# Kernel tuning notes

Hardware: AMD Instinct MI355X
Metric: run time of the kernel (lower is better)

## Reference

```python
import jax, jax.numpy as jnp
import numpy as np

D = 4096   # dim_context == dim_hid
A = 10     # dim_out (agent feature vector)
EPS = 1e-5


def _ln(x, g, b):
    mu = jnp.mean(x)
    var = jnp.mean((x - mu) ** 2)
    return (x - mu) / jnp.sqrt(var + EPS) * g + b


def _mlp3(x, W0, b0, g0, be0, W1, b1, g1, be1, W2, b2):
    # Linear -> LayerNorm -> ReLU, twice, then final Linear
    h = jax.nn.relu(_ln(W0 @ x + b0, g0, be0))
    h = jax.nn.relu(_ln(W1 @ h + b1, g1, be1))
    return W2 @ h + b2


def _lin_init(key, d_out, d_in):
    s = 1.0 / np.sqrt(d_in)
    return jax.random.uniform(key, (d_out, d_in), jnp.float32, -s, s)


def setup_inputs() -> dict:
    key = jax.random.key(0)
    ks = jax.random.split(key, 24)
    inp = {
        "context_vec": jax.random.normal(ks[0], (D,), jnp.float32),
        "prev_hidden": jax.random.normal(ks[1], (D,), jnp.float32),
        "attn_scores": jax.random.normal(ks[2], (D,), jnp.float32),
        "prev_agent_feat": jax.random.normal(ks[3], (A,), jnp.float32),
        # input_mlp: (A+D) -> D -> D -> D
        "in_W0": _lin_init(ks[4], D, A + D), "in_b0": jnp.zeros((D,), jnp.float32),
        "in_g0": jnp.ones((D,), jnp.float32), "in_be0": jnp.zeros((D,), jnp.float32),
        "in_W1": _lin_init(ks[5], D, D), "in_b1": jnp.zeros((D,), jnp.float32),
        "in_g1": jnp.ones((D,), jnp.float32), "in_be1": jnp.zeros((D,), jnp.float32),
        "in_W2": _lin_init(ks[6], D, D), "in_b2": jnp.zeros((D,), jnp.float32),
        # GRUCell (gate order: r, z, n)
        "gru_Wih": _lin_init(ks[7], 3 * D, D), "gru_Whh": _lin_init(ks[8], 3 * D, D),
        "gru_bih": jnp.zeros((3 * D,), jnp.float32), "gru_bhh": jnp.zeros((3 * D,), jnp.float32),
        # out_mlp: D -> D -> D -> A
        "out_W0": _lin_init(ks[9], D, D), "out_b0": jnp.zeros((D,), jnp.float32),
        "out_g0": jnp.ones((D,), jnp.float32), "out_be0": jnp.zeros((D,), jnp.float32),
        "out_W1": _lin_init(ks[10], D, D), "out_b1": jnp.zeros((D,), jnp.float32),
        "out_g1": jnp.ones((D,), jnp.float32), "out_be1": jnp.zeros((D,), jnp.float32),
        "out_W2": _lin_init(ks[11], A, D), "out_b2": jnp.zeros((A,), jnp.float32),
    }
    return inp


def _forward(context_vec, prev_hidden, attn_scores, prev_agent_feat,
             in_W0, in_b0, in_g0, in_be0, in_W1, in_b1, in_g1, in_be1, in_W2, in_b2,
             gru_Wih, gru_Whh, gru_bih, gru_bhh,
             out_W0, out_b0, out_g0, out_be0, out_W1, out_b1, out_g1, out_be1, out_W2, out_b2):
    attn_w = jax.nn.softmax(attn_scores)
    gru_in = jnp.concatenate([attn_w * context_vec, prev_agent_feat])  # [D+A]
    gru_in = jax.nn.relu(_mlp3(gru_in, in_W0, in_b0, in_g0, in_be0,
                               in_W1, in_b1, in_g1, in_be1, in_W2, in_b2))
    # GRUCell
    gi = gru_Wih @ gru_in + gru_bih
    gh = gru_Whh @ prev_hidden + gru_bhh
    r = jax.nn.sigmoid(gi[:D] + gh[:D])
    z = jax.nn.sigmoid(gi[D:2 * D] + gh[D:2 * D])
    n = jnp.tanh(gi[2 * D:] + r * gh[2 * D:])
    hidden = (1.0 - z) * n + z * prev_hidden
    out = _mlp3(hidden, out_W0, out_b0, out_g0, out_be0,
                out_W1, out_b1, out_g1, out_be1, out_W2, out_b2)
    agent_feat = jnp.concatenate([
        out[0:2],
        out[2:4] / jnp.linalg.norm(out[2:4]),
        jax.nn.softplus(out[4:7]),
        jax.nn.softmax(out[7:10]),
    ])
    return agent_feat, hidden


def reference(context_vec, prev_hidden, attn_scores, prev_agent_feat,
              in_W0, in_b0, in_g0, in_be0, in_W1, in_b1, in_g1, in_be1, in_W2, in_b2,
              gru_Wih, gru_Whh, gru_bih, gru_bhh,
              out_W0, out_b0, out_g0, out_be0, out_W1, out_b1, out_g1, out_be1, out_W2, out_b2):
    return _forward(context_vec, prev_hidden, attn_scores, prev_agent_feat,
                    in_W0, in_b0, in_g0, in_be0, in_W1, in_b1, in_g1, in_be1, in_W2, in_b2,
                    gru_Wih, gru_Whh, gru_bih, gru_bhh,
                    out_W0, out_b0, out_g0, out_be0, out_W1, out_b1, out_g1, out_be1, out_W2, out_b2)
```

## Files before the change

### kernel.cpp

```cpp
#include <hip/hip_runtime.h>
#include <math.h>

#define D 4096
#define DA 4106

__device__ __forceinline__ float wave_reduce_sum(float v) {
    #pragma unroll
    for (int off = 32; off > 0; off >>= 1) v += __shfl_xor(v, off, 64);
    return v;
}
__device__ __forceinline__ float wave_reduce_max(float v) {
    #pragma unroll
    for (int off = 32; off > 0; off >>= 1) v = fmaxf(v, __shfl_xor(v, off, 64));
    return v;
}

__global__ __launch_bounds__(1024)
void prep_kernel(const float* __restrict__ attn, const float* __restrict__ ctx,
                 const float* __restrict__ paf, float* __restrict__ gin) {
    __shared__ float red[16];
    __shared__ float bmax, bsum;
    int tid = threadIdx.x, wave = tid >> 6, lane = tid & 63;

    float4 a = ((const float4*)attn)[tid];
    float mx = fmaxf(fmaxf(a.x, a.y), fmaxf(a.z, a.w));
    mx = wave_reduce_max(mx);
    if (lane == 0) red[wave] = mx;
    __syncthreads();
    if (tid == 0) {
        float m = red[0];
        #pragma unroll
        for (int k = 1; k < 16; ++k) m = fmaxf(m, red[k]);
        bmax = m;
    }
    __syncthreads();
    mx = bmax;

    float e0 = expf(a.x - mx), e1 = expf(a.y - mx), e2 = expf(a.z - mx), e3 = expf(a.w - mx);
    float s = wave_reduce_sum(e0 + e1 + e2 + e3);
    __syncthreads();
    if (lane == 0) red[wave] = s;
    __syncthreads();
    if (tid == 0) {
        float t = 0.f;
        #pragma unroll
        for (int k = 0; k < 16; ++k) t += red[k];
        bsum = t;
    }
    __syncthreads();
    float inv = 1.f / bsum;

    float4 c = ((const float4*)ctx)[tid];
    float4 o;
    o.x = e0 * inv * c.x; o.y = e1 * inv * c.y; o.z = e2 * inv * c.z; o.w = e3 * inv * c.w;
    ((float4*)gin)[tid] = o;
    if (tid < 10) gin[D + tid] = paf[tid];
}

template<int NC, bool LN_IN, bool RELU_OUT, int RPW>
__global__ __launch_bounds__(256)
void gemv_kernel(const float* __restrict__ W, const float* __restrict__ xin,
                 const float* __restrict__ bias,
                 const float* __restrict__ g, const float* __restrict__ be,
                 float* __restrict__ y) {
    __shared__ float xs[4160];
    __shared__ float red[8];
    int tid = threadIdx.x, wave = tid >> 6, lane = tid & 63;

    if constexpr (LN_IN) {
        const float4* x4 = (const float4*)xin;
        float4 vals[4];
        float s1 = 0.f, s2 = 0.f;
        #pragma unroll
        for (int k = 0; k < 4; ++k) {
            float4 v = x4[tid + k * 256];
            vals[k] = v;
            s1 += (v.x + v.y) + (v.z + v.w);
            s2 += (v.x * v.x + v.y * v.y) + (v.z * v.z + v.w * v.w);
        }
        s1 = wave_reduce_sum(s1); s2 = wave_reduce_sum(s2);
        if (lane == 0) { red[wave] = s1; red[4 + wave] = s2; }
        __syncthreads();
        float ts1 = (red[0] + red[1]) + (red[2] + red[3]);
        float ts2 = (red[4] + red[5]) + (red[6] + red[7]);
        float mu = ts1 * (1.f / 4096.f);
        float rstd = rsqrtf(ts2 * (1.f / 4096.f) - mu * mu + 1e-5f);
        #pragma unroll
        for (int k = 0; k < 4; ++k) {
            float4 v = vals[k];
            float4 gg = ((const float4*)g)[tid + k * 256];
            float4 bb = ((const float4*)be)[tid + k * 256];
            float4 o;
            o.x = fmaxf((v.x - mu) * rstd * gg.x + bb.x, 0.f);
            o.y = fmaxf((v.y - mu) * rstd * gg.y + bb.y, 0.f);
            o.z = fmaxf((v.z - mu) * rstd * gg.z + bb.z, 0.f);
            o.w = fmaxf((v.w - mu) * rstd * gg.w + bb.w, 0.f);
            ((float4*)xs)[tid + k * 256] = o;
        }
        __syncthreads();
    } else {
        for (int i = tid; i < (NC >> 1); i += 256)
            ((float2*)xs)[i] = ((const float2*)xin)[i];
        __syncthreads();
    }

    int row0 = (blockIdx.x * 4 + wave) * RPW;
    if constexpr ((NC & 255) == 0) {
        constexpr int NIT = NC >> 8;
        const float4* xs4 = (const float4*)xs;
        for (int rr = 0; rr < RPW; ++rr) {
            int row = row0 + rr;
            const float4* Wr = (const float4*)(W + (size_t)row * NC);
            float ax = 0.f, ay = 0.f, az = 0.f, aw = 0.f;
            #pragma unroll 8
            for (int it = 0; it < NIT; ++it) {
                float4 w = Wr[it * 64 + lane];
                float4 xv = xs4[it * 64 + lane];
                ax += w.x * xv.x; ay += w.y * xv.y; az += w.z * xv.z; aw += w.w * xv.w;
            }
            float s = wave_reduce_sum((ax + ay) + (az + aw));
            if (lane == 0) {
                s += bias[row];
                if (RELU_OUT) s = fmaxf(s, 0.f);
                y[row] = s;
            }
        }
    } else {
        constexpr int NC2 = NC >> 1;
        constexpr int NFULL = NC2 >> 6;
        const float2* xs2 = (const float2*)xs;
        for (int rr = 0; rr < RPW; ++rr) {
            int row = row0 + rr;
            const float2* Wr = (const float2*)(W + (size_t)row * NC);
            float ax = 0.f, ay = 0.f;
            #pragma unroll 8
            for (int it = 0; it < NFULL; ++it) {
                float2 w = Wr[it * 64 + lane];
                float2 xv = xs2[it * 64 + lane];
                ax += w.x * xv.x; ay += w.y * xv.y;
            }
            int idx = (NFULL << 6) + lane;
            if (idx < NC2) {
                float2 w = Wr[idx];
                float2 xv = xs2[idx];
                ax += w.x * xv.x; ay += w.y * xv.y;
            }
            float s = wave_reduce_sum(ax + ay);
            if (lane == 0) {
                s += bias[row];
                if (RELU_OUT) s = fmaxf(s, 0.f);
                y[row] = s;
            }
        }
    }
}

template<int RPW>
__global__ __launch_bounds__(256)
void gru_gemv_kernel(const float* __restrict__ Wih, const float* __restrict__ Whh,
                     const float* __restrict__ xa, const float* __restrict__ xb,
                     const float* __restrict__ bih, const float* __restrict__ bhh,
                     float* __restrict__ gi, float* __restrict__ gh) {
    __shared__ float xsa[D], xsb[D];
    int tid = threadIdx.x, wave = tid >> 6, lane = tid & 63;
    for (int i = tid; i < 1024; i += 256) {
        ((float4*)xsa)[i] = ((const float4*)xa)[i];
        ((float4*)xsb)[i] = ((const float4*)xb)[i];
    }
    __syncthreads();

    const float4* xa4 = (const float4*)xsa;
    const float4* xb4 = (const float4*)xsb;
    int row0 = (blockIdx.x * 4 + wave) * RPW;
    for (int rr = 0; rr < RPW; ++rr) {
        int row = row0 + rr;
        {
            const float4* Wr = (const float4*)(Wih + (size_t)row * D);
            float ax = 0.f, ay = 0.f, az = 0.f, aw = 0.f;
            #pragma unroll 8
            for (int it = 0; it < 16; ++it) {
                float4 w = Wr[it * 64 + lane];
                float4 xv = xa4[it * 64 + lane];
                ax += w.x * xv.x; ay += w.y * xv.y; az += w.z * xv.z; aw += w.w * xv.w;
            }
            float s = wave_reduce_sum((ax + ay) + (az + aw));
            if (lane == 0) gi[row] = s + bih[row];
        }
        {
            const float4* Wr = (const float4*)(Whh + (size_t)row * D);
            float ax = 0.f, ay = 0.f, az = 0.f, aw = 0.f;
            #pragma unroll 8
            for (int it = 0; it < 16; ++it) {
                float4 w = Wr[it * 64 + lane];
                float4 xv = xb4[it * 64 + lane];
                ax += w.x * xv.x; ay += w.y * xv.y; az += w.z * xv.z; aw += w.w * xv.w;
            }
            float s = wave_reduce_sum((ax + ay) + (az + aw));
            if (lane == 0) gh[row] = s + bhh[row];
        }
    }
}

__global__ __launch_bounds__(256)
void gru_combine_kernel(const float* __restrict__ gi, const float* __restrict__ gh,
                        const float* __restrict__ hprev,
                        float* __restrict__ hidden, float* __restrict__ out_hidden) {
    int j = blockIdx.x * 256 + threadIdx.x;
    float r = 1.f / (1.f + expf(-(gi[j] + gh[j])));
    float z = 1.f / (1.f + expf(-(gi[D + j] + gh[D + j])));
    float n = tanhf(gi[2 * D + j] + r * gh[2 * D + j]);
    float h = (1.f - z) * n + z * hprev[j];
    hidden[j] = h;
    out_hidden[j] = h;
}

__global__ __launch_bounds__(1024)
void final_kernel(const float* __restrict__ t4, const float* __restrict__ g,
                  const float* __restrict__ be, const float* __restrict__ W2,
                  const float* __restrict__ b2, float* __restrict__ dout) {
    __shared__ float xs[D];
    __shared__ float red[32];
    __shared__ float out10[10];
    int tid = threadIdx.x, wave = tid >> 6, lane = tid & 63;

    float4 v = ((const float4*)t4)[tid];
    float s1 = (v.x + v.y) + (v.z + v.w);
    float s2 = (v.x * v.x + v.y * v.y) + (v.z * v.z + v.w * v.w);
    s1 = wave_reduce_sum(s1); s2 = wave_reduce_sum(s2);
    if (lane == 0) { red[wave] = s1; red[16 + wave] = s2; }
    __syncthreads();
    float ts1 = 0.f, ts2 = 0.f;
    #pragma unroll
    for (int k = 0; k < 16; ++k) { ts1 += red[k]; ts2 += red[16 + k]; }
    float mu = ts1 * (1.f / 4096.f);
    float rstd = rsqrtf(ts2 * (1.f / 4096.f) - mu * mu + 1e-5f);
    float4 gg = ((const float4*)g)[tid], bb = ((const float4*)be)[tid];
    float4 o;
    o.x = fmaxf((v.x - mu) * rstd * gg.x + bb.x, 0.f);
    o.y = fmaxf((v.y - mu) * rstd * gg.y + bb.y, 0.f);
    o.z = fmaxf((v.z - mu) * rstd * gg.z + bb.z, 0.f);
    o.w = fmaxf((v.w - mu) * rstd * gg.w + bb.w, 0.f);
    ((float4*)xs)[tid] = o;
    __syncthreads();

    if (wave < 10) {
        const float4* Wr = (const float4*)(W2 + (size_t)wave * D);
        const float4* xs4 = (const float4*)xs;
        float ax = 0.f, ay = 0.f, az = 0.f, aw = 0.f;
        #pragma unroll
        for (int it = 0; it < 16; ++it) {
            float4 w = Wr[it * 64 + lane];
            float4 xv = xs4[it * 64 + lane];
            ax += w.x * xv.x; ay += w.y * xv.y; az += w.z * xv.z; aw += w.w * xv.w;
        }
        float s = wave_reduce_sum((ax + ay) + (az + aw));
        if (lane == 0) out10[wave] = s + b2[wave];
    }
    __syncthreads();

    if (tid == 0) {
        dout[0] = out10[0];
        dout[1] = out10[1];
        float nr = sqrtf(out10[2] * out10[2] + out10[3] * out10[3]);
        dout[2] = out10[2] / nr;
        dout[3] = out10[3] / nr;
        #pragma unroll
        for (int k = 4; k < 7; ++k) {
            float x = out10[k];
            dout[k] = fmaxf(x, 0.f) + log1pf(expf(-fabsf(x)));
        }
        float m = fmaxf(out10[7], fmaxf(out10[8], out10[9]));
        float e7 = expf(out10[7] - m), e8 = expf(out10[8] - m), e9 = expf(out10[9] - m);
        float inv = 1.f / (e7 + e8 + e9);
        dout[7] = e7 * inv; dout[8] = e8 * inv; dout[9] = e9 * inv;
    }
}

extern "C" void kernel_launch(void* const* d_in, const int* in_sizes, int n_in,
                              void* d_out, int out_size, void* d_ws, size_t ws_size,
                              hipStream_t stream) {
    const float* ctx     = (const float*)d_in[0];
    const float* hprev   = (const float*)d_in[1];
    const float* attn    = (const float*)d_in[2];
    const float* paf     = (const float*)d_in[3];
    const float* in_W0   = (const float*)d_in[4];
    const float* in_b0   = (const float*)d_in[5];
    const float* in_g0   = (const float*)d_in[6];
    const float* in_be0  = (const float*)d_in[7];
    const float* in_W1   = (const float*)d_in[8];
    const float* in_b1   = (const float*)d_in[9];
    const float* in_g1   = (const float*)d_in[10];
    const float* in_be1  = (const float*)d_in[11];
    const float* in_W2   = (const float*)d_in[12];
    const float* in_b2   = (const float*)d_in[13];
    const float* gru_Wih = (const float*)d_in[14];
    const float* gru_Whh = (const float*)d_in[15];
    const float* gru_bih = (const float*)d_in[16];
    const float* gru_bhh = (const float*)d_in[17];
    const float* out_W0  = (const float*)d_in[18];
    const float* out_b0  = (const float*)d_in[19];
    const float* out_g0  = (const float*)d_in[20];
    const float* out_be0 = (const float*)d_in[21];
    const float* out_W1  = (const float*)d_in[22];
    const float* out_b1  = (const float*)d_in[23];
    const float* out_g1  = (const float*)d_in[24];
    const float* out_be1 = (const float*)d_in[25];
    const float* out_W2  = (const float*)d_in[26];
    const float* out_b2  = (const float*)d_in[27];

    float* out = (float*)d_out;
    float* ws  = (float*)d_ws;

    float* gin = ws;
    float* t0  = ws + 4160;
    float* t1  = ws + 8256;
    float* gx  = ws + 12352;
    float* gi  = ws + 16448;
    float* gh  = ws + 28736;
    float* hid = ws + 41024;
    float* t3  = ws + 45120;
    float* t4  = ws + 49216;

    prep_kernel<<<1, 1024, 0, stream>>>(attn, ctx, paf, gin);
    gemv_kernel<DA, false, false, 2><<<512, 256, 0, stream>>>(in_W0, gin, in_b0, nullptr, nullptr, t0);
    gemv_kernel<D,  true,  false, 2><<<512, 256, 0, stream>>>(in_W1, t0, in_b1, in_g0, in_be0, t1);
    gemv_kernel<D,  true,  true,  2><<<512, 256, 0, stream>>>(in_W2, t1, in_b2, in_g1, in_be1, gx);
    gru_gemv_kernel<2><<<1536, 256, 0, stream>>>(gru_Wih, gru_Whh, gx, hprev,
                                                 gru_bih, gru_bhh, gi, gh);
    gru_combine_kernel<<<16, 256, 0, stream>>>(gi, gh, hprev, hid, out + 10);
    gemv_kernel<D, false, false, 2><<<512, 256, 0, stream>>>(out_W0, hid, out_b0, nullptr, nullptr, t3);
    gemv_kernel<D, true,  false, 2><<<512, 256, 0, stream>>>(out_W1, t3, out_b1, out_g0, out_be0, t4);
    final_kernel<<<1, 1024, 0, stream>>>(t4, out_g1, out_be1, out_W2, out_b2, out);
}
```

Before: 651.6 us.

## Switch GEMVs to one row per block with registers instead of LDS staging

```diff
diff --git a/kernel.cpp b/kernel.cpp
--- a/kernel.cpp
+++ b/kernel.cpp
@@ -57,24 +57,26 @@
     if (tid < 10) gin[D + tid] = paf[tid];
 }
 
-template<int NC, bool LN_IN, bool RELU_OUT, int RPW>
-__global__ __launch_bounds__(256)
-void gemv_kernel(const float* __restrict__ W, const float* __restrict__ xin,
-                 const float* __restrict__ bias,
-                 const float* __restrict__ g, const float* __restrict__ be,
-                 float* __restrict__ y) {
-    __shared__ float xs[4160];
+template<bool LN_IN, bool RELU_OUT>
+__global__ __launch_bounds__(256, LN_IN ? 6 : 8)
+void gemv_row_kernel(const float* __restrict__ W, const float* __restrict__ xin,
+                     const float* __restrict__ bias,
+                     const float* __restrict__ g, const float* __restrict__ be,
+                     float* __restrict__ y) {
     __shared__ float red[8];
     int tid = threadIdx.x, wave = tid >> 6, lane = tid & 63;
+    int row = blockIdx.x;
+
+    const float4* x4 = (const float4*)xin;
+    float4 xv[4];
+    #pragma unroll
+    for (int k = 0; k < 4; ++k) xv[k] = x4[k * 256 + tid];
 
     if constexpr (LN_IN) {
-        const float4* x4 = (const float4*)xin;
-        float4 vals[4];
         float s1 = 0.f, s2 = 0.f;
         #pragma unroll
         for (int k = 0; k < 4; ++k) {
-            float4 v = x4[tid + k * 256];
-            vals[k] = v;
+            float4 v = xv[k];
             s1 += (v.x + v.y) + (v.z + v.w);
             s2 += (v.x * v.x + v.y * v.y) + (v.z * v.z + v.w * v.w);
         }
@@ -87,118 +89,89 @@
         float rstd = rsqrtf(ts2 * (1.f / 4096.f) - mu * mu + 1e-5f);
         #pragma unroll
         for (int k = 0; k < 4; ++k) {
-            float4 v = vals[k];
-            float4 gg = ((const float4*)g)[tid + k * 256];
-            float4 bb = ((const float4*)be)[tid + k * 256];
-            float4 o;
-            o.x = fmaxf((v.x - mu) * rstd * gg.x + bb.x, 0.f);
-            o.y = fmaxf((v.y - mu) * rstd * gg.y + bb.y, 0.f);
-            o.z = fmaxf((v.z - mu) * rstd * gg.z + bb.z, 0.f);
-            o.w = fmaxf((v.w - mu) * rstd * gg.w + bb.w, 0.f);
-            ((float4*)xs)[tid + k * 256] = o;
+            float4 v = xv[k];
+            float4 gg = ((const float4*)g)[k * 256 + tid];
+            float4 bb = ((const float4*)be)[k * 256 + tid];
+            v.x = fmaxf((v.x - mu) * rstd * gg.x + bb.x, 0.f);
+            v.y = fmaxf((v.y - mu) * rstd * gg.y + bb.y, 0.f);
+            v.z = fmaxf((v.z - mu) * rstd * gg.z + bb.z, 0.f);
+            v.w = fmaxf((v.w - mu) * rstd * gg.w + bb.w, 0.f);
+            xv[k] = v;
         }
-        __syncthreads();
-    } else {
-        for (int i = tid; i < (NC >> 1); i += 256)
-            ((float2*)xs)[i] = ((const float2*)xin)[i];
-        __syncthreads();
-    }
-
-    int row0 = (blockIdx.x * 4 + wave) * RPW;
-    if constexpr ((NC & 255) == 0) {
-        constexpr int NIT = NC >> 8;
-        const float4* xs4 = (const float4*)xs;
-        for (int rr = 0; rr < RPW; ++rr) {
-            int row = row0 + rr;
-            const float4* Wr = (const float4*)(W + (size_t)row * NC);
-            float ax = 0.f, ay = 0.f, az = 0.f, aw = 0.f;
-            #pragma unroll 8
-            for (int it = 0; it < NIT; ++it) {
-                float4 w = Wr[it * 64 + lane];
-                float4 xv = xs4[it * 64 + lane];
-                ax += w.x * xv.x; ay += w.y * xv.y; az += w.z * xv.z; aw += w.w * xv.w;
-            }
-            float s = wave_reduce_sum((ax + ay) + (az + aw));
-            if (lane == 0) {
-                s += bias[row];
-                if (RELU_OUT) s = fmaxf(s, 0.f);
-                y[row] = s;
-            }
-        }
-    } else {
-        constexpr int NC2 = NC >> 1;
-        constexpr int NFULL = NC2 >> 6;
-        const float2* xs2 = (const float2*)xs;
-        for (int rr = 0; rr < RPW; ++rr) {
-            int row = row0 + rr;
-            const float2* Wr = (const float2*)(W + (size_t)row * NC);
-            float ax = 0.f, ay = 0.f;
-            #pragma unroll 8
-            for (int it = 0; it < NFULL; ++it) {
-                float2 w = Wr[it * 64 + lane];
-                float2 xv = xs2[it * 64 + lane];
-                ax += w.x * xv.x; ay += w.y * xv.y;
-            }
-            int idx = (NFULL << 6) + lane;
-            if (idx < NC2) {
-                float2 w = Wr[idx];
-                float2 xv = xs2[idx];
-                ax += w.x * xv.x; ay += w.y * xv.y;
-            }
-            float s = wave_reduce_sum(ax + ay);
-            if (lane == 0) {
-                s += bias[row];
-                if (RELU_OUT) s = fmaxf(s, 0.f);
-                y[row] = s;
-            }
-        }
-    }
-}
-
-template<int RPW>
-__global__ __launch_bounds__(256)
+    }
+
+    const float4* Wr = (const float4*)(W + (size_t)row * D);
+    float4 wv[4];
+    #pragma unroll
+    for (int k = 0; k < 4; ++k) wv[k] = Wr[k * 256 + tid];
+    float acc = 0.f;
+    #pragma unroll
+    for (int k = 0; k < 4; ++k)
+        acc += (wv[k].x * xv[k].x + wv[k].y * xv[k].y) +
+               (wv[k].z * xv[k].z + wv[k].w * xv[k].w);
+    acc = wave_reduce_sum(acc);
+
+    __syncthreads();
+    if (lane == 0) red[wave] = acc;
+    __syncthreads();
+    if (tid == 0) {
+        float s = (red[0] + red[1]) + (red[2] + red[3]) + bias[row];
+        if (RELU_OUT) s = fmaxf(s, 0.f);
+        y[row] = s;
+    }
+}
+
+__global__ __launch_bounds__(256, 8)
+void gemv_w0_kernel(const float* __restrict__ W, const float* __restrict__ xin,
+                    const float* __restrict__ bias, float* __restrict__ y) {
+    __shared__ float red[4];
+    int tid = threadIdx.x, wave = tid >> 6, lane = tid & 63;
+    int row = blockIdx.x;
+
+    const float2* x2 = (const float2*)xin;
+    const float2* Wr = (const float2*)(W + (size_t)row * DA);
+    float2 xv[8], wv[8];
+    #pragma unroll
+    for (int k = 0; k < 8; ++k) { xv[k] = x2[k * 256 + tid]; wv[k] = Wr[k * 256 + tid]; }
+    float acc = 0.f;
+    #pragma unroll
+    for (int k = 0; k < 8; ++k) acc += wv[k].x * xv[k].x + wv[k].y * xv[k].y;
+    if (tid < 5) {
+        float2 xt = x2[2048 + tid], wt = Wr[2048 + tid];
+        acc += wt.x * xt.x + wt.y * xt.y;
+    }
+    acc = wave_reduce_sum(acc);
+    if (lane == 0) red[wave] = acc;
+    __syncthreads();
+    if (tid == 0) y[row] = (red[0] + red[1]) + (red[2] + red[3]) + bias[row];
+}
+
+__global__ __launch_bounds__(256, 8)
 void gru_gemv_kernel(const float* __restrict__ Wih, const float* __restrict__ Whh,
                      const float* __restrict__ xa, const float* __restrict__ xb,
                      const float* __restrict__ bih, const float* __restrict__ bhh,
                      float* __restrict__ gi, float* __restrict__ gh) {
-    __shared__ float xsa[D], xsb[D];
-    int tid = threadIdx.x, wave = tid >> 6, lane = tid & 63;
-    for (int i = tid; i < 1024; i += 256) {
-        ((float4*)xsa)[i] = ((const float4*)xa)[i];
-        ((float4*)xsb)[i] = ((const float4*)xb)[i];
-    }
-    __syncthreads();
-
-    const float4* xa4 = (const float4*)xsa;
-    const float4* xb4 = (const float4*)xsb;
-    int row0 = (blockIdx.x * 4 + wave) * RPW;
-    for (int rr = 0; rr < RPW; ++rr) {
-        int row = row0 + rr;
-        {
-            const float4* Wr = (const float4*)(Wih + (size_t)row * D);
-            float ax = 0.f, ay = 0.f, az = 0.f, aw = 0.f;
-            #pragma unroll 8
-            for (int it = 0; it < 16; ++it) {
-                float4 w = Wr[it * 64 + lane];
-                float4 xv = xa4[it * 64 + lane];
-                ax += w.x * xv.x; ay += w.y * xv.y; az += w.z * xv.z; aw += w.w * xv.w;
-            }
-            float s = wave_reduce_sum((ax + ay) + (az + aw));
-            if (lane == 0) gi[row] = s + bih[row];
-        }
-        {
-            const float4* Wr = (const float4*)(Whh + (size_t)row * D);
-            float ax = 0.f, ay = 0.f, az = 0.f, aw = 0.f;
-            #pragma unroll 8
-            for (int it = 0; it < 16; ++it) {
-                float4 w = Wr[it * 64 + lane];
-                float4 xv = xb4[it * 64 + lane];
-                ax += w.x * xv.x; ay += w.y * xv.y; az += w.z * xv.z; aw += w.w * xv.w;
-            }
-            float s = wave_reduce_sum((ax + ay) + (az + aw));
-            if (lane == 0) gh[row] = s + bhh[row];
-        }
-    }
+    __shared__ float red[4];
+    int b = blockIdx.x;
+    int tid = threadIdx.x, wave = tid >> 6, lane = tid & 63;
+    const float* W; const float* x; const float* bias; float* y; int row;
+    if (b < 12288) { W = Wih; x = xa; bias = bih; y = gi; row = b; }
+    else           { W = Whh; x = xb; bias = bhh; y = gh; row = b - 12288; }
+
+    const float4* x4 = (const float4*)x;
+    const float4* Wr = (const float4*)(W + (size_t)row * D);
+    float4 xv[4], wv[4];
+    #pragma unroll
+    for (int k = 0; k < 4; ++k) { xv[k] = x4[k * 256 + tid]; wv[k] = Wr[k * 256 + tid]; }
+    float acc = 0.f;
+    #pragma unroll
+    for (int k = 0; k < 4; ++k)
+        acc += (wv[k].x * xv[k].x + wv[k].y * xv[k].y) +
+               (wv[k].z * xv[k].z + wv[k].w * xv[k].w);
+    acc = wave_reduce_sum(acc);
+    if (lane == 0) red[wave] = acc;
+    __syncthreads();
+    if (tid == 0) y[row] = (red[0] + red[1]) + (red[2] + red[3]) + bias[row];
 }
 
 __global__ __launch_bounds__(256)
@@ -322,13 +295,13 @@
     float* t4  = ws + 49216;
 
     prep_kernel<<<1, 1024, 0, stream>>>(attn, ctx, paf, gin);
-    gemv_kernel<DA, false, false, 2><<<512, 256, 0, stream>>>(in_W0, gin, in_b0, nullptr, nullptr, t0);
-    gemv_kernel<D,  true,  false, 2><<<512, 256, 0, stream>>>(in_W1, t0, in_b1, in_g0, in_be0, t1);
-    gemv_kernel<D,  true,  true,  2><<<512, 256, 0, stream>>>(in_W2, t1, in_b2, in_g1, in_be1, gx);
-    gru_gemv_kernel<2><<<1536, 256, 0, stream>>>(gru_Wih, gru_Whh, gx, hprev,
-                                                 gru_bih, gru_bhh, gi, gh);
+    gemv_w0_kernel<<<4096, 256, 0, stream>>>(in_W0, gin, in_b0, t0);
+    gemv_row_kernel<true,  false><<<4096, 256, 0, stream>>>(in_W1, t0, in_b1, in_g0, in_be0, t1);
+    gemv_row_kernel<true,  true ><<<4096, 256, 0, stream>>>(in_W2, t1, in_b2, in_g1, in_be1, gx);
+    gru_gemv_kernel<<<24576, 256, 0, stream>>>(gru_Wih, gru_Whh, gx, hprev,
+                                               gru_bih, gru_bhh, gi, gh);
     gru_combine_kernel<<<16, 256, 0, stream>>>(gi, gh, hprev, hid, out + 10);
-    gemv_kernel<D, false, false, 2><<<512, 256, 0, stream>>>(out_W0, hid, out_b0, nullptr, nullptr, t3);
-    gemv_kernel<D, true,  false, 2><<<512, 256, 0, stream>>>(out_W1, t3, out_b1, out_g0, out_be0, t4);
+    gemv_row_kernel<false, false><<<4096, 256, 0, stream>>>(out_W0, hid, out_b0, nullptr, nullptr, t3);
+    gemv_row_kernel<true,  false><<<4096, 256, 0, stream>>>(out_W1, t3, out_b1, out_g0, out_be0, t4);
     final_kernel<<<1, 1024, 0, stream>>>(t4, out_g1, out_be1, out_W2, out_b2, out);
 }
```

Result: faster. 638.7 us (-2.0%).
